# Kernel optimization log

Hardware: AMD Instinct MI355X
Metric: run time of the kernel (lower is better)

The kernel has to match this reference:

```python
import jax, jax.numpy as jnp
import numpy as np

TEMPERATURE = 0.07
NUM_NEGATIVES = 128
B, C, H, W = 4, 256, 32, 32
N_TOTAL = B * H * W  # 4096


def setup_inputs() -> dict:
    key = jax.random.key(0)
    k1, k2, k3 = jax.random.split(key, 3)
    feat_q = jax.random.normal(k1, (B, C, H, W), dtype=jnp.float32)
    feat_k = jax.random.normal(k2, (B, C, H, W), dtype=jnp.float32)
    # uniform draws in [0, N_TOTAL-1): same distribution as indexing into the
    # length-(N-1) 'choices' array in the original per-i loop
    neg_indices = jax.random.randint(k3, (N_TOTAL, NUM_NEGATIVES), 0, N_TOTAL - 1, dtype=jnp.int64 if jax.config.jax_enable_x64 else jnp.int32)
    return {"feat_q": feat_q, "feat_k": feat_k, "neg_indices": neg_indices}


def reference(feat_q, feat_k, neg_indices):
    b, c, h, w = feat_q.shape
    n = b * h * w
    q = feat_q.reshape(b, c, -1)
    k = feat_k.reshape(b, c, -1)
    # F.normalize(dim=1), eps=1e-12
    q = q / jnp.maximum(jnp.linalg.norm(q, axis=1, keepdims=True), 1e-12)
    k = k / jnp.maximum(jnp.linalg.norm(k, axis=1, keepdims=True), 1e-12)
    q = q.transpose(0, 2, 1).reshape(-1, c)  # [N, C]
    k = k.transpose(0, 2, 1).reshape(-1, c)  # [N, C]
    l_pos = jnp.sum(q * k, axis=1, keepdims=True)  # [N, 1]
    # self-exclusion: choices = all_idx without i -> shift sampled idx >= i up by 1
    row = jnp.arange(n, dtype=neg_indices.dtype)[:, None]
    idx = neg_indices + (neg_indices >= row).astype(neg_indices.dtype)  # [N, K]
    k_neg = k[idx]  # [N, K, C] gather
    l_neg = jnp.einsum('nc,nkc->nk', q, k_neg)  # [N, K]
    logits = jnp.concatenate([l_pos, l_neg], axis=1) / TEMPERATURE  # [N, 1+K]
    # cross-entropy with label 0 for every row
    loss = jnp.mean(jax.nn.logsumexp(logits, axis=1) - logits[:, 0])
    return loss
```

## Files before the change

kernel.cpp:

```cpp
#include <hip/hip_runtime.h>
#include <hip/hip_bf16.h>

#define N_TOTAL 4096
#define C_DIM 256
#define K_NEG 128
#define HW 1024
#define TEMP_INV (1.0f / 0.07f)

typedef _Float16 h8 __attribute__((ext_vector_type(8)));
typedef _Float16 h2 __attribute__((ext_vector_type(2)));

__global__ __launch_bounds__(256) void norm_tr_kernel(
    const float* __restrict__ fq, const float* __restrict__ fk,
    _Float16* __restrict__ qh, _Float16* __restrict__ kh) {
  const int bid = blockIdx.x;
  const int tensor = bid >> 8;
  const int chunk = bid & 255;
  const int n0 = chunk * 16;
  const int b = n0 / HW, s0 = n0 % HW;
  const float* base = (tensor ? fk : fq) + (size_t)b * C_DIM * HW + s0;
  _Float16* out = tensor ? kh : qh;
  const float scale_extra = tensor ? 1.0f : TEMP_INV;

  const int t = threadIdx.x;
  __shared__ float tile[16][C_DIM + 1];
  __shared__ float red[16][17];
  __shared__ float sinv[16];

  {
    const float* src = base + (size_t)t * HW;
#pragma unroll
    for (int p = 0; p < 4; ++p) {
      const float4 v = *(const float4*)(src + p * 4);
      tile[p * 4 + 0][t] = v.x;
      tile[p * 4 + 1][t] = v.y;
      tile[p * 4 + 2][t] = v.z;
      tile[p * 4 + 3][t] = v.w;
    }
  }
  __syncthreads();

  {
    const int s = t & 15, cg = t >> 4;
    float acc = 0.f;
#pragma unroll
    for (int i = 0; i < 16; ++i) {
      float v = tile[s][cg * 16 + i];
      acc = fmaf(v, v, acc);
    }
    red[s][cg] = acc;
  }
  __syncthreads();
  if (t < 16) {
    float tot = 0.f;
#pragma unroll
    for (int g = 0; g < 16; ++g) tot += red[t][g];
    sinv[t] = scale_extra / fmaxf(sqrtf(tot), 1e-12f);
  }
  __syncthreads();

  {
    const int s = t & 15, c16 = t >> 4;
    const float inv = sinv[s];
    h8 o0, o1;
#pragma unroll
    for (int j = 0; j < 8; ++j) o0[j] = (_Float16)(tile[s][c16 * 16 + j] * inv);
#pragma unroll
    for (int j = 0; j < 8; ++j)
      o1[j] = (_Float16)(tile[s][c16 * 16 + 8 + j] * inv);
    h8* dst = (h8*)(out + (size_t)(n0 + s) * C_DIM + c16 * 16);
    dst[0] = o0;
    dst[1] = o1;
  }
}

__global__ __launch_bounds__(512, 4) void nce_kernel(
    const _Float16* __restrict__ qh, const _Float16* __restrict__ kh,
    const int* __restrict__ neg, float* __restrict__ loss_buf) {
  const int tid = threadIdx.x;
  const int w = tid >> 6, lane = tid & 63;
  const int sub = lane & 7;
  const int unit = lane >> 3;
  const int n = blockIdx.x * 8 + w;

  union H { h8 v; h2 p[4]; };

  const h8* qrow = (const h8*)(qh + (size_t)n * C_DIM);
  h8 qv[4];
#pragma unroll
  for (int i = 0; i < 4; ++i) qv[i] = qrow[i * 8 + sub];
  const h8* kpr = (const h8*)(kh + (size_t)n * C_DIM);
  h8 kp[4];
#pragma unroll
  for (int i = 0; i < 4; ++i) kp[i] = kpr[i * 8 + sub];

  const int* nrow = neg + (size_t)n * K_NEG + unit * 16;

  float m = -1e30f, s = 0.f;
#pragma unroll 2
  for (int j = 0; j < 16; ++j) {
    const int x = nrow[j];
    const int r = x + (x >= n ? 1 : 0);
    const h8* kr = (const h8*)(kh + (size_t)r * C_DIM);
    float a0 = 0.f, a1 = 0.f;
#pragma unroll
    for (int i = 0; i < 4; ++i) {
      H a; a.v = qv[i];
      H b; b.v = kr[i * 8 + sub];
      a0 = __builtin_amdgcn_fdot2(b.p[0], a.p[0], a0, false);
      a1 = __builtin_amdgcn_fdot2(b.p[1], a.p[1], a1, false);
      a0 = __builtin_amdgcn_fdot2(b.p[2], a.p[2], a0, false);
      a1 = __builtin_amdgcn_fdot2(b.p[3], a.p[3], a1, false);
    }
    float acc = a0 + a1;
    acc += __shfl_xor(acc, 1);
    acc += __shfl_xor(acc, 2);
    acc += __shfl_xor(acc, 4);
    const float mn = fmaxf(m, acc);
    s = s * __expf(m - mn) + __expf(acc - mn);
    m = mn;
  }

  float lp;
  {
    float a0 = 0.f, a1 = 0.f;
#pragma unroll
    for (int i = 0; i < 4; ++i) {
      H a; a.v = qv[i];
      H b; b.v = kp[i];
      a0 = __builtin_amdgcn_fdot2(b.p[0], a.p[0], a0, false);
      a1 = __builtin_amdgcn_fdot2(b.p[1], a.p[1], a1, false);
      a0 = __builtin_amdgcn_fdot2(b.p[2], a.p[2], a0, false);
      a1 = __builtin_amdgcn_fdot2(b.p[3], a.p[3], a1, false);
    }
    float acc = a0 + a1;
    acc += __shfl_xor(acc, 1);
    acc += __shfl_xor(acc, 2);
    acc += __shfl_xor(acc, 4);
    lp = acc;
  }

#pragma unroll
  for (int off = 8; off <= 32; off <<= 1) {
    const float mo = __shfl_xor(m, off);
    const float so = __shfl_xor(s, off);
    const float mn = fmaxf(m, mo);
    s = s * __expf(m - mn) + so * __expf(mo - mn);
    m = mn;
  }
  const float M = fmaxf(m, lp);
  const float stot = s * __expf(m - M) + __expf(lp - M);
  if (lane == 0) loss_buf[n] = M + __logf(stot) - lp;
}

__global__ __launch_bounds__(1024) void reduce_kernel(
    const float* __restrict__ loss_buf, float* __restrict__ out) {
  const int t = threadIdx.x;
  const float4 v = ((const float4*)loss_buf)[t];
  float s = (v.x + v.y) + (v.z + v.w);
#pragma unroll
  for (int off = 32; off; off >>= 1) s += __shfl_xor(s, off);
  __shared__ float red[16];
  if ((t & 63) == 0) red[t >> 6] = s;
  __syncthreads();
  if (t < 16) {
    float x = red[t];
#pragma unroll
    for (int off = 8; off; off >>= 1) x += __shfl_xor(x, off);
    if (t == 0) out[0] = x * (1.0f / N_TOTAL);
  }
}

extern "C" void kernel_launch(void* const* d_in, const int* in_sizes, int n_in,
                              void* d_out, int out_size, void* d_ws,
                              size_t ws_size, hipStream_t stream) {
  const float* fq = (const float*)d_in[0];
  const float* fk = (const float*)d_in[1];
  const int* neg = (const int*)d_in[2];
  float* out = (float*)d_out;

  _Float16* qh = (_Float16*)d_ws;
  _Float16* kh = qh + (size_t)N_TOTAL * C_DIM;
  float* loss_buf = (float*)(kh + (size_t)N_TOTAL * C_DIM);

  hipLaunchKernelGGL(norm_tr_kernel, dim3(512), dim3(256), 0, stream,
                     fq, fk, qh, kh);
  hipLaunchKernelGGL(nce_kernel, dim3(N_TOTAL / 8), dim3(512), 0, stream,
                     qh, kh, neg, loss_buf);
  hipLaunchKernelGGL(reduce_kernel, dim3(1), dim3(1024), 0, stream,
                     loss_buf, out);
}
```

Before: 80.99 us.

## Fuse normalize, NCE, and reduction into one cooperative kernel with grid sync

Merges the three kernels into a single cooperative launch of 256 blocks. Each block normalizes two 16-row chunks, performs a grid-wide sync, computes the NCE loss for 16 rows, syncs again, and block 0 does the final mean. The aim is to remove two kernel launch boundaries and their gaps. The cost is two grid barriers and only 256 blocks for the gather phase, which lowers occupancy and latency hiding compared with the previous 512-block NCE launch.

Result: slower. 149.7 us (+84.8%).

```diff
diff --git a/kernel.cpp b/kernel.cpp
--- a/kernel.cpp
+++ b/kernel.cpp
@@ -1,5 +1,8 @@
 #include <hip/hip_runtime.h>
 #include <hip/hip_bf16.h>
+#include <hip/hip_cooperative_groups.h>
+
+namespace cg = cooperative_groups;
 
 #define N_TOTAL 4096
 #define C_DIM 256
@@ -10,164 +13,177 @@
 typedef _Float16 h8 __attribute__((ext_vector_type(8)));
 typedef _Float16 h2 __attribute__((ext_vector_type(2)));
 
-__global__ __launch_bounds__(256) void norm_tr_kernel(
+__global__ __launch_bounds__(512, 2) void fused_kernel(
     const float* __restrict__ fq, const float* __restrict__ fk,
-    _Float16* __restrict__ qh, _Float16* __restrict__ kh) {
+    const int* __restrict__ neg, _Float16* __restrict__ qh,
+    _Float16* __restrict__ kh, float* __restrict__ loss_buf,
+    float* __restrict__ out) {
+  const int t = threadIdx.x;
   const int bid = blockIdx.x;
-  const int tensor = bid >> 8;
-  const int chunk = bid & 255;
-  const int n0 = chunk * 16;
-  const int b = n0 / HW, s0 = n0 % HW;
-  const float* base = (tensor ? fk : fq) + (size_t)b * C_DIM * HW + s0;
-  _Float16* out = tensor ? kh : qh;
-  const float scale_extra = tensor ? 1.0f : TEMP_INV;
-
-  const int t = threadIdx.x;
-  __shared__ float tile[16][C_DIM + 1];
-  __shared__ float red[16][17];
-  __shared__ float sinv[16];
+
+  __shared__ float tile[2][16][C_DIM + 1];
+  __shared__ float red[2][16][17];
+  __shared__ float sinv[2][16];
+  __shared__ float red3[8];
 
   {
-    const float* src = base + (size_t)t * HW;
-#pragma unroll
-    for (int p = 0; p < 4; ++p) {
-      const float4 v = *(const float4*)(src + p * 4);
-      tile[p * 4 + 0][t] = v.x;
-      tile[p * 4 + 1][t] = v.y;
-      tile[p * 4 + 2][t] = v.z;
-      tile[p * 4 + 3][t] = v.w;
+    const int g = t >> 8, u = t & 255;
+    const int cid = bid * 2 + g;
+    const int tensor = cid >> 8;
+    const int chunk = cid & 255;
+    const int n0 = chunk * 16;
+    const int b = n0 / HW, s0 = n0 % HW;
+    const float* base = (tensor ? fk : fq) + (size_t)b * C_DIM * HW + s0;
+    _Float16* outp = tensor ? kh : qh;
+    const float scale_extra = tensor ? 1.0f : TEMP_INV;
+
+    {
+      const float* src = base + (size_t)u * HW;
+#pragma unroll
+      for (int p = 0; p < 4; ++p) {
+        const float4 v = *(const float4*)(src + p * 4);
+        tile[g][p * 4 + 0][u] = v.x;
+        tile[g][p * 4 + 1][u] = v.y;
+        tile[g][p * 4 + 2][u] = v.z;
+        tile[g][p * 4 + 3][u] = v.w;
+      }
+    }
+    __syncthreads();
+
+    {
+      const int s = u & 15, cg16 = u >> 4;
+      float acc = 0.f;
+#pragma unroll
+      for (int i = 0; i < 16; ++i) {
+        float v = tile[g][s][cg16 * 16 + i];
+        acc = fmaf(v, v, acc);
+      }
+      red[g][s][cg16] = acc;
+    }
+    __syncthreads();
+    if (u < 16) {
+      float tot = 0.f;
+#pragma unroll
+      for (int j = 0; j < 16; ++j) tot += red[g][u][j];
+      sinv[g][u] = scale_extra / fmaxf(sqrtf(tot), 1e-12f);
+    }
+    __syncthreads();
+
+    {
+      const int s = u & 15, c16 = u >> 4;
+      const float inv = sinv[g][s];
+      h8 o0, o1;
+#pragma unroll
+      for (int j = 0; j < 8; ++j)
+        o0[j] = (_Float16)(tile[g][s][c16 * 16 + j] * inv);
+#pragma unroll
+      for (int j = 0; j < 8; ++j)
+        o1[j] = (_Float16)(tile[g][s][c16 * 16 + 8 + j] * inv);
+      h8* dst = (h8*)(outp + (size_t)(n0 + s) * C_DIM + c16 * 16);
+      dst[0] = o0;
+      dst[1] = o1;
     }
   }
-  __syncthreads();
+
+  cg::this_grid().sync();
 
   {
-    const int s = t & 15, cg = t >> 4;
-    float acc = 0.f;
-#pragma unroll
-    for (int i = 0; i < 16; ++i) {
-      float v = tile[s][cg * 16 + i];
-      acc = fmaf(v, v, acc);
-    }
-    red[s][cg] = acc;
+    const int w = t >> 6, lane = t & 63;
+    const int sub = lane & 7;
+    const int unit = lane >> 3;
+
+    union H { h8 v; h2 p[4]; };
+
+#pragma unroll
+    for (int rr = 0; rr < 2; ++rr) {
+      const int n = bid * 16 + rr * 8 + w;
+
+      const h8* qrow = (const h8*)(qh + (size_t)n * C_DIM);
+      h8 qv[4];
+#pragma unroll
+      for (int i = 0; i < 4; ++i) qv[i] = qrow[i * 8 + sub];
+      const h8* kpr = (const h8*)(kh + (size_t)n * C_DIM);
+      h8 kp[4];
+#pragma unroll
+      for (int i = 0; i < 4; ++i) kp[i] = kpr[i * 8 + sub];
+
+      const int* nrow = neg + (size_t)n * K_NEG + unit * 16;
+
+      float m = -1e30f, s = 0.f;
+#pragma unroll 4
+      for (int j = 0; j < 16; ++j) {
+        const int x = nrow[j];
+        const int r = x + (x >= n ? 1 : 0);
+        const h8* kr = (const h8*)(kh + (size_t)r * C_DIM);
+        float a0 = 0.f, a1 = 0.f;
+#pragma unroll
+        for (int i = 0; i < 4; ++i) {
+          H a; a.v = qv[i];
+          H b; b.v = kr[i * 8 + sub];
+          a0 = __builtin_amdgcn_fdot2(b.p[0], a.p[0], a0, false);
+          a1 = __builtin_amdgcn_fdot2(b.p[1], a.p[1], a1, false);
+          a0 = __builtin_amdgcn_fdot2(b.p[2], a.p[2], a0, false);
+          a1 = __builtin_amdgcn_fdot2(b.p[3], a.p[3], a1, false);
+        }
+        float acc = a0 + a1;
+        acc += __shfl_xor(acc, 1);
+        acc += __shfl_xor(acc, 2);
+        acc += __shfl_xor(acc, 4);
+        const float mn = fmaxf(m, acc);
+        s = s * __expf(m - mn) + __expf(acc - mn);
+        m = mn;
+      }
+
+      float lp;
+      {
+        float a0 = 0.f, a1 = 0.f;
+#pragma unroll
+        for (int i = 0; i < 4; ++i) {
+          H a; a.v = qv[i];
+          H b; b.v = kp[i];
+          a0 = __builtin_amdgcn_fdot2(b.p[0], a.p[0], a0, false);
+          a1 = __builtin_amdgcn_fdot2(b.p[1], a.p[1], a1, false);
+          a0 = __builtin_amdgcn_fdot2(b.p[2], a.p[2], a0, false);
+          a1 = __builtin_amdgcn_fdot2(b.p[3], a.p[3], a1, false);
+        }
+        float acc = a0 + a1;
+        acc += __shfl_xor(acc, 1);
+        acc += __shfl_xor(acc, 2);
+        acc += __shfl_xor(acc, 4);
+        lp = acc;
+      }
+
+#pragma unroll
+      for (int off = 8; off <= 32; off <<= 1) {
+        const float mo = __shfl_xor(m, off);
+        const float so = __shfl_xor(s, off);
+        const float mn = fmaxf(m, mo);
+        s = s * __expf(m - mn) + so * __expf(mo - mn);
+        m = mn;
+      }
+      const float M = fmaxf(m, lp);
+      const float stot = s * __expf(m - M) + __expf(lp - M);
+      if (lane == 0) loss_buf[n] = M + __logf(stot) - lp;
+    }
   }
-  __syncthreads();
-  if (t < 16) {
-    float tot = 0.f;
-#pragma unroll
-    for (int g = 0; g < 16; ++g) tot += red[t][g];
-    sinv[t] = scale_extra / fmaxf(sqrtf(tot), 1e-12f);
-  }
-  __syncthreads();
-
-  {
-    const int s = t & 15, c16 = t >> 4;
-    const float inv = sinv[s];
-    h8 o0, o1;
-#pragma unroll
-    for (int j = 0; j < 8; ++j) o0[j] = (_Float16)(tile[s][c16 * 16 + j] * inv);
-#pragma unroll
-    for (int j = 0; j < 8; ++j)
-      o1[j] = (_Float16)(tile[s][c16 * 16 + 8 + j] * inv);
-    h8* dst = (h8*)(out + (size_t)(n0 + s) * C_DIM + c16 * 16);
-    dst[0] = o0;
-    dst[1] = o1;
-  }
-}
-
-__global__ __launch_bounds__(512, 4) void nce_kernel(
-    const _Float16* __restrict__ qh, const _Float16* __restrict__ kh,
-    const int* __restrict__ neg, float* __restrict__ loss_buf) {
-  const int tid = threadIdx.x;
-  const int w = tid >> 6, lane = tid & 63;
-  const int sub = lane & 7;
-  const int unit = lane >> 3;
-  const int n = blockIdx.x * 8 + w;
-
-  union H { h8 v; h2 p[4]; };
-
-  const h8* qrow = (const h8*)(qh + (size_t)n * C_DIM);
-  h8 qv[4];
-#pragma unroll
-  for (int i = 0; i < 4; ++i) qv[i] = qrow[i * 8 + sub];
-  const h8* kpr = (const h8*)(kh + (size_t)n * C_DIM);
-  h8 kp[4];
-#pragma unroll
-  for (int i = 0; i < 4; ++i) kp[i] = kpr[i * 8 + sub];
-
-  const int* nrow = neg + (size_t)n * K_NEG + unit * 16;
-
-  float m = -1e30f, s = 0.f;
-#pragma unroll 2
-  for (int j = 0; j < 16; ++j) {
-    const int x = nrow[j];
-    const int r = x + (x >= n ? 1 : 0);
-    const h8* kr = (const h8*)(kh + (size_t)r * C_DIM);
-    float a0 = 0.f, a1 = 0.f;
-#pragma unroll
-    for (int i = 0; i < 4; ++i) {
-      H a; a.v = qv[i];
-      H b; b.v = kr[i * 8 + sub];
-      a0 = __builtin_amdgcn_fdot2(b.p[0], a.p[0], a0, false);
-      a1 = __builtin_amdgcn_fdot2(b.p[1], a.p[1], a1, false);
-      a0 = __builtin_amdgcn_fdot2(b.p[2], a.p[2], a0, false);
-      a1 = __builtin_amdgcn_fdot2(b.p[3], a.p[3], a1, false);
-    }
-    float acc = a0 + a1;
-    acc += __shfl_xor(acc, 1);
-    acc += __shfl_xor(acc, 2);
-    acc += __shfl_xor(acc, 4);
-    const float mn = fmaxf(m, acc);
-    s = s * __expf(m - mn) + __expf(acc - mn);
-    m = mn;
-  }
-
-  float lp;
-  {
-    float a0 = 0.f, a1 = 0.f;
-#pragma unroll
-    for (int i = 0; i < 4; ++i) {
-      H a; a.v = qv[i];
-      H b; b.v = kp[i];
-      a0 = __builtin_amdgcn_fdot2(b.p[0], a.p[0], a0, false);
-      a1 = __builtin_amdgcn_fdot2(b.p[1], a.p[1], a1, false);
-      a0 = __builtin_amdgcn_fdot2(b.p[2], a.p[2], a0, false);
-      a1 = __builtin_amdgcn_fdot2(b.p[3], a.p[3], a1, false);
-    }
-    float acc = a0 + a1;
-    acc += __shfl_xor(acc, 1);
-    acc += __shfl_xor(acc, 2);
-    acc += __shfl_xor(acc, 4);
-    lp = acc;
-  }
-
-#pragma unroll
-  for (int off = 8; off <= 32; off <<= 1) {
-    const float mo = __shfl_xor(m, off);
-    const float so = __shfl_xor(s, off);
-    const float mn = fmaxf(m, mo);
-    s = s * __expf(m - mn) + so * __expf(mo - mn);
-    m = mn;
-  }
-  const float M = fmaxf(m, lp);
-  const float stot = s * __expf(m - M) + __expf(lp - M);
-  if (lane == 0) loss_buf[n] = M + __logf(stot) - lp;
-}
-
-__global__ __launch_bounds__(1024) void reduce_kernel(
-    const float* __restrict__ loss_buf, float* __restrict__ out) {
-  const int t = threadIdx.x;
-  const float4 v = ((const float4*)loss_buf)[t];
-  float s = (v.x + v.y) + (v.z + v.w);
-#pragma unroll
-  for (int off = 32; off; off >>= 1) s += __shfl_xor(s, off);
-  __shared__ float red[16];
-  if ((t & 63) == 0) red[t >> 6] = s;
-  __syncthreads();
-  if (t < 16) {
-    float x = red[t];
-#pragma unroll
-    for (int off = 8; off; off >>= 1) x += __shfl_xor(x, off);
-    if (t == 0) out[0] = x * (1.0f / N_TOTAL);
+
+  cg::this_grid().sync();
+
+  if (bid == 0) {
+    const float4 v0 = ((const float4*)loss_buf)[2 * t];
+    const float4 v1 = ((const float4*)loss_buf)[2 * t + 1];
+    float s = ((v0.x + v0.y) + (v0.z + v0.w)) +
+              ((v1.x + v1.y) + (v1.z + v1.w));
+#pragma unroll
+    for (int off = 32; off; off >>= 1) s += __shfl_xor(s, off);
+    if ((t & 63) == 0) red3[t >> 6] = s;
+    __syncthreads();
+    if (t < 8) {
+      float x = red3[t];
+#pragma unroll
+      for (int off = 4; off; off >>= 1) x += __shfl_xor(x, off);
+      if (t == 0) out[0] = x * (1.0f / N_TOTAL);
+    }
   }
 }
 
@@ -183,10 +199,8 @@
   _Float16* kh = qh + (size_t)N_TOTAL * C_DIM;
   float* loss_buf = (float*)(kh + (size_t)N_TOTAL * C_DIM);
 
-  hipLaunchKernelGGL(norm_tr_kernel, dim3(512), dim3(256), 0, stream,
-                     fq, fk, qh, kh);
-  hipLaunchKernelGGL(nce_kernel, dim3(N_TOTAL / 8), dim3(512), 0, stream,
-                     qh, kh, neg, loss_buf);
-  hipLaunchKernelGGL(reduce_kernel, dim3(1), dim3(1024), 0, stream,
-                     loss_buf, out);
+  void* args[] = {(void*)&fq, (void*)&fk, (void*)&neg, (void*)&qh,
+                  (void*)&kh, (void*)&loss_buf, (void*)&out};
+  hipLaunchCooperativeKernel((const void*)fused_kernel, dim3(256), dim3(512),
+                             args, 0, stream);
 }
```
